# Kernel tuning notes

Hardware: AMD Instinct MI355X
Metric: run time of the kernel (lower is better)

The kernel has to match this reference:

```python
import jax, jax.numpy as jnp
import numpy as np

N = 131072      # nodes decoded per call
LAT, REP, H = 64, 128, 256
FEAT, CEMB, NMAP, CNUM = 512, 128, 101, 27
TEMP = 0.5


def setup_inputs() -> dict:
    key = jax.random.key(0)
    ks = iter(jax.random.split(key, 40))
    w = lambda shape: jax.random.normal(next(ks), shape, jnp.float32) * 0.02
    inp = {
        "z": jax.random.normal(next(ks), (N, LAT), jnp.float32),
        "cluster_ind": jax.random.randint(next(ks), (N,), 0, CNUM),
        "Emb": w((CNUM, CEMB)),
        "Wld": w((LAT, REP)), "bld": w((REP,)),
        "Wrd": w((REP, 3 * H)), "brd": w((3 * H,)),
        "Wfd": w((H, FEAT)), "bfd": w((FEAT,)),
        "Wc1": w((H, H)), "bc1": w((H,)),
        "Wc2": w((H, H)), "bc2": w((H,)),
        "Wc3": w((H, H)), "bc3": w((H,)),
        "Wcd": w((H, CNUM)), "bcd": w((CNUM,)),
        "Wcn": w((CEMB, H)), "bcn": w((H,)),
        "Wnd": w((H, 2 * H)), "bnd": w((2 * H,)),
        "Wn1": w((2 * H, 2 * H)), "bn1": w((2 * H,)),
        "Wn2": w((2 * H, 2 * H)), "bn2": w((2 * H,)),
        "Wa0": w((2 * H, 4 * H)), "ba0": w((4 * H,)),
        "Wa1": w((4 * H, 2 * H)), "ba1": w((2 * H,)),
        "Wn3": w((2 * H, NMAP)), "bn3": w((NMAP,)),
    }
    return inp


def reference(z, cluster_ind, Emb, Wld, bld, Wrd, brd, Wfd, bfd,
              Wc1, bc1, Wc2, bc2, Wc3, bc3, Wcd, bcd, Wcn, bcn,
              Wnd, bnd, Wn1, bn1, Wn2, bn2, Wa0, ba0, Wa1, ba1, Wn3, bn3):
    relu = jax.nn.relu
    # latent -> reparam -> hidden*3, chunked into (feat, neighbor, cluster)
    z1 = relu(z @ Wld + bld)
    z2 = relu(z1 @ Wrd + brd)
    feat_h, nb_h, cl_h = jnp.split(z2, 3, axis=-1)  # each [N, H]
    # feature head
    feat = jax.nn.sigmoid(feat_h @ Wfd + bfd)
    # cluster head
    c = relu(cl_h @ Wc1 + bc1)
    c = relu(c @ Wc2 + bc2)
    c = relu(c @ Wc3 + bc3)
    cluster = jax.nn.sigmoid((c @ Wcd + bcd) / TEMP)
    # neighbor head, conditioned on cluster embedding (training branch)
    emb = Emb[cluster_ind]                      # [N, CEMB]
    ctn = relu(emb @ Wcn + bcn)                 # [N, H]
    nf = relu((nb_h + ctn) @ Wnd + bnd)
    nf = relu(nf @ Wn1 + bn1)
    nf = relu(nf @ Wn2 + bn2)
    nf = relu(nf @ Wa0 + ba0)
    nf = relu(nf @ Wa1 + ba1)
    neighbor_map = jax.nn.sigmoid((nf @ Wn3 + bn3) / TEMP)
    return (feat, neighbor_map, cluster)
```

## Files before the change

### kernel.cpp

```cpp
#include <hip/hip_runtime.h>
#include <hip/hip_bf16.h>

typedef short bf16x8 __attribute__((ext_vector_type(8)));
typedef float f32x4 __attribute__((ext_vector_type(4)));

#define NN 131072
#define BM 128
#define WRS 512
#define SRS 128

#define OFF_LD 0
#define OFF_RD 8192
#define OFF_FD 106496
#define OFF_C1 237568
#define OFF_C2 303104
#define OFF_C3 368640
#define OFF_CD 434176
#define OFF_CN 442368
#define OFF_ND 475136
#define OFF_N1 606208
#define OFF_N2 868352
#define OFF_A0 1130496
#define OFF_A1 1654784
#define OFF_N3 2179072
#define WT_TOTAL 2236416

__device__ __forceinline__ unsigned short f2b(float f) {
  __hip_bfloat16 h = __float2bfloat16(f);
  return __builtin_bit_cast(unsigned short, h);
}
__device__ __forceinline__ float b2f(unsigned short u) {
  return __bfloat162float(__builtin_bit_cast(__hip_bfloat16, u));
}

template<int Kd, int Md>
__device__ __forceinline__ unsigned short convF(int local, const float* __restrict__ W) {
  int block = local >> 9;
  int within = local & 511;
  int lane = within >> 3, j = within & 7;
  constexpr int NK = Kd / 32;
  int ctile = block / NK;
  int kch = block - ctile * NK;
  int col = ctile * 16 + (lane & 15);
  int k = kch * 32 + (lane >> 4) * 8 + j;
  return (col < Md) ? f2b(W[(size_t)k * Md + col]) : (unsigned short)0;
}

__global__ void prep_weights(const float* __restrict__ Wld, const float* __restrict__ Wrd,
                             const float* __restrict__ Wfd, const float* __restrict__ Wc1,
                             const float* __restrict__ Wc2, const float* __restrict__ Wc3,
                             const float* __restrict__ Wcd, const float* __restrict__ Wcn,
                             const float* __restrict__ Wnd, const float* __restrict__ Wn1,
                             const float* __restrict__ Wn2, const float* __restrict__ Wa0,
                             const float* __restrict__ Wa1, const float* __restrict__ Wn3,
                             unsigned short* __restrict__ WT) {
  int e = blockIdx.x * 256 + threadIdx.x;
  unsigned short r;
  if      (e < OFF_RD) r = convF<64, 128>(e - OFF_LD, Wld);
  else if (e < OFF_FD) r = convF<128, 768>(e - OFF_RD, Wrd);
  else if (e < OFF_C1) r = convF<256, 512>(e - OFF_FD, Wfd);
  else if (e < OFF_C2) r = convF<256, 256>(e - OFF_C1, Wc1);
  else if (e < OFF_C3) r = convF<256, 256>(e - OFF_C2, Wc2);
  else if (e < OFF_CD) r = convF<256, 256>(e - OFF_C3, Wc3);
  else if (e < OFF_CN) r = convF<256, 27>(e - OFF_CD, Wcd);
  else if (e < OFF_ND) r = convF<128, 256>(e - OFF_CN, Wcn);
  else if (e < OFF_N1) r = convF<256, 512>(e - OFF_ND, Wnd);
  else if (e < OFF_N2) r = convF<512, 512>(e - OFF_N1, Wn1);
  else if (e < OFF_A0) r = convF<512, 512>(e - OFF_N2, Wn2);
  else if (e < OFF_A1) r = convF<512, 1024>(e - OFF_A0, Wa0);
  else if (e < OFF_N3) r = convF<1024, 512>(e - OFF_A1, Wa1);
  else                 r = convF<512, 101>(e - OFF_N3, Wn3);
  WT[e] = r;
}

template<int K, int NOUT, int GSIZE, int ACT, bool TO_GLOBAL, bool ADD>
__device__ __forceinline__ void layer(
    const unsigned short* __restrict__ Ain, int ars,
    const unsigned short* __restrict__ Bw,
    const float* __restrict__ bias,
    unsigned short* __restrict__ Lout, int ors,
    float* __restrict__ Gout, int gld,
    const unsigned short* __restrict__ Aadd, int rsa,
    int lane, int wid) {
  constexpr int NS = K / 32;
  constexpr int NT = (NOUT + 15) >> 4;
  constexpr int NG = (NT + GSIZE - 1) / GSIZE;
  const int cg = wid >> 1;
  const int rbase = (wid & 1) * 64;
  const int l15 = lane & 15;
  const int quad = lane >> 4;
  const int kh = quad << 3;
  const int sw = (l15 & 7) << 3;
  const unsigned short* ab = Ain + (rbase + l15) * ars;
  #pragma unroll 1
  for (int g = cg; g < NG; g += 4) {
    f32x4 acc[4][GSIZE] = {};
    const unsigned short* bp[GSIZE];
    #pragma unroll
    for (int t = 0; t < GSIZE; ++t) {
      int ti = g * GSIZE + t;
      int tc = ti < NT ? ti : NT - 1;
      bp[t] = Bw + (size_t)tc * (NS * 512) + lane * 8;
    }
    __builtin_amdgcn_s_setprio(1);
    #pragma unroll 2
    for (int s = 0; s < NS; ++s) {
      bf16x8 bb[GSIZE];
      #pragma unroll
      for (int t = 0; t < GSIZE; ++t) bb[t] = *(const bf16x8*)(bp[t] + s * 512);
      int kx = (kh + s * 32) ^ sw;
      #pragma unroll
      for (int m = 0; m < 4; ++m) {
        bf16x8 a = *(const bf16x8*)(ab + m * 16 * ars + kx);
        #pragma unroll
        for (int t = 0; t < GSIZE; ++t)
          acc[m][t] = __builtin_amdgcn_mfma_f32_16x16x32_bf16(a, bb[t], acc[m][t], 0, 0, 0);
      }
    }
    __builtin_amdgcn_s_setprio(0);
    #pragma unroll
    for (int t = 0; t < GSIZE; ++t) {
      int col = (g * GSIZE + t) * 16 + l15;
      int cc = col < NOUT ? col : NOUT - 1;
      float bb2 = bias[cc];
      #pragma unroll
      for (int m = 0; m < 4; ++m) {
        #pragma unroll
        for (int j = 0; j < 4; ++j) {
          int row = rbase + m * 16 + quad * 4 + j;
          int rsw = (row & 7) << 3;
          float v = acc[m][t][j] + bb2;
          if constexpr (ACT == 0) v = fmaxf(v, 0.f);
          else if constexpr (ACT == 1) v = 1.f / (1.f + __expf(-v));
          else if constexpr (ACT == 2) v = 1.f / (1.f + __expf(-2.f * v));
          if constexpr (ADD) v += b2f(Aadd[row * rsa + (col ^ rsw)]);
          if constexpr (TO_GLOBAL) {
            if (col < NOUT) Gout[(size_t)row * gld + col] = v;
          } else {
            Lout[row * ors + (col ^ rsw)] = f2b(v);
          }
        }
      }
    }
  }
}

template<int K>
__device__ __forceinline__ void layer512_ip(
    unsigned short* __restrict__ Wb,
    const unsigned short* __restrict__ Bw, const float* __restrict__ bias,
    int lane, int wid) {
  constexpr int NS = K / 32;
  const int cg = wid >> 1;
  const int rbase = (wid & 1) * 64;
  const int l15 = lane & 15;
  const int quad = lane >> 4;
  const int kh = quad << 3;
  const int sw = (l15 & 7) << 3;
  f32x4 acc[4][8] = {};
  const unsigned short* bp = Bw + (size_t)(cg * 8) * (NS * 512) + lane * 8;
  const unsigned short* ab = Wb + (rbase + l15) * WRS;
  __builtin_amdgcn_s_setprio(1);
  #pragma unroll 2
  for (int s = 0; s < NS; ++s) {
    bf16x8 bb[8];
    #pragma unroll
    for (int t = 0; t < 8; ++t) bb[t] = *(const bf16x8*)(bp + (size_t)t * (NS * 512) + s * 512);
    int kx = (kh + s * 32) ^ sw;
    #pragma unroll
    for (int m = 0; m < 4; ++m) {
      bf16x8 a = *(const bf16x8*)(ab + m * 16 * WRS + kx);
      #pragma unroll
      for (int t = 0; t < 8; ++t)
        acc[m][t] = __builtin_amdgcn_mfma_f32_16x16x32_bf16(a, bb[t], acc[m][t], 0, 0, 0);
    }
  }
  __builtin_amdgcn_s_setprio(0);
  __syncthreads();
  #pragma unroll
  for (int t = 0; t < 8; ++t) {
    int col = cg * 128 + t * 16 + l15;
    float bb2 = bias[col];
    #pragma unroll
    for (int m = 0; m < 4; ++m) {
      #pragma unroll
      for (int j = 0; j < 4; ++j) {
        int row = rbase + m * 16 + quad * 4 + j;
        Wb[row * WRS + (col ^ ((row & 7) << 3))] = f2b(fmaxf(acc[m][t][j] + bb2, 0.f));
      }
    }
  }
  __syncthreads();
}

__global__ __launch_bounds__(512, 2)
void fused_vae(const float* __restrict__ z, const int* __restrict__ cind,
               const float* __restrict__ Emb,
               const float* __restrict__ bld, const float* __restrict__ brd,
               const float* __restrict__ bfd, const float* __restrict__ bc1,
               const float* __restrict__ bc2, const float* __restrict__ bc3,
               const float* __restrict__ bcd, const float* __restrict__ bcn,
               const float* __restrict__ bnd, const float* __restrict__ bn1,
               const float* __restrict__ bn2, const float* __restrict__ ba0,
               const float* __restrict__ ba1, const float* __restrict__ bn3,
               const unsigned short* __restrict__ WT, float* __restrict__ out) {
  __shared__ unsigned short lds[BM * (WRS + SRS)];
  unsigned short* Wb = lds;
  unsigned short* Sb = lds + BM * WRS;
  const int tid = threadIdx.x;
  const int lane = tid & 63;
  const int wid = tid >> 6;
  const size_t row0 = (size_t)blockIdx.x * BM;

  for (int e = tid * 4; e < BM * 64; e += 512 * 4) {
    int r = e >> 6, c = e & 63;
    float4 v = *(const float4*)(z + (row0 + r) * 64 + c);
    ushort4 u; u.x = f2b(v.x); u.y = f2b(v.y); u.z = f2b(v.z); u.w = f2b(v.w);
    *(ushort4*)(&Wb[r * WRS + (c ^ ((r & 7) << 3))]) = u;
  }
  __syncthreads();
  layer<64, 128, 2, 0, false, false>(Wb, WRS, WT + OFF_LD, bld, Sb, SRS, nullptr, 0, nullptr, 0, lane, wid);
  __syncthreads();
  layer<128, 256, 4, 0, false, false>(Sb, SRS, WT + OFF_RD + (size_t)32 * 4 * 512, brd + 512, Wb, WRS, nullptr, 0, nullptr, 0, lane, wid);
  __syncthreads();
  layer<256, 256, 4, 0, false, false>(Wb, WRS, WT + OFF_C1, bc1, Wb + 256, WRS, nullptr, 0, nullptr, 0, lane, wid);
  __syncthreads();
  layer<256, 256, 4, 0, false, false>(Wb + 256, WRS, WT + OFF_C2, bc2, Wb, WRS, nullptr, 0, nullptr, 0, lane, wid);
  __syncthreads();
  layer<256, 256, 4, 0, false, false>(Wb, WRS, WT + OFF_C3, bc3, Wb + 256, WRS, nullptr, 0, nullptr, 0, lane, wid);
  __syncthreads();
  layer<256, 27, 1, 2, true, false>(Wb + 256, WRS, WT + OFF_CD, bcd, nullptr, 0,
                                    out + (size_t)NN * 613 + row0 * 27, 27, nullptr, 0, lane, wid);
  layer<128, 256, 4, 0, false, false>(Sb, SRS, WT + OFF_RD, brd, Wb, WRS, nullptr, 0, nullptr, 0, lane, wid);
  __syncthreads();
  layer<256, 512, 4, 1, true, false>(Wb, WRS, WT + OFF_FD, bfd, nullptr, 0,
                                     out + row0 * 512, 512, nullptr, 0, lane, wid);
  layer<128, 256, 4, 0, false, false>(Sb, SRS, WT + OFF_RD + (size_t)16 * 4 * 512, brd + 256, Wb + 256, WRS, nullptr, 0, nullptr, 0, lane, wid);
  __syncthreads();
  for (int e = tid * 4; e < BM * 128; e += 512 * 4) {
    int r = e >> 7, c = e & 127;
    int ci = cind[row0 + r];
    float4 v = *(const float4*)(Emb + (size_t)ci * 128 + c);
    ushort4 u; u.x = f2b(v.x); u.y = f2b(v.y); u.z = f2b(v.z); u.w = f2b(v.w);
    *(ushort4*)(&Sb[r * SRS + (c ^ ((r & 7) << 3))]) = u;
  }
  __syncthreads();
  layer<128, 256, 4, 0, false, true>(Sb, SRS, WT + OFF_CN, bcn, Wb, WRS, nullptr, 0, Wb + 256, WRS, lane, wid);
  __syncthreads();
  layer512_ip<256>(Wb, WT + OFF_ND, bnd, lane, wid);
  layer512_ip<512>(Wb, WT + OFF_N1, bn1, lane, wid);
  layer512_ip<512>(Wb, WT + OFF_N2, bn2, lane, wid);
  {
    const int l15 = lane & 15;
    const int quad = lane >> 4;
    const int kh = quad << 3;
    const int sw = (l15 & 7) << 3;
    #pragma unroll 1
    for (int rh = 0; rh < 2; ++rh) {
      f32x4 acc1[4][4] = {};
      const unsigned short* awb = Wb + (rh * 64 + l15) * WRS;
      const unsigned short* asb = Sb + l15 * 256;
      #pragma unroll 1
      for (int e = 0; e < 4; ++e) {
        f32x4 acc0[4][2] = {};
        const unsigned short* bp0 = WT + OFF_A0 + (size_t)(e * 16 + wid * 2) * (16 * 512) + lane * 8;
        __builtin_amdgcn_s_setprio(1);
        #pragma unroll 2
        for (int s = 0; s < 16; ++s) {
          bf16x8 b0 = *(const bf16x8*)(bp0 + s * 512);
          bf16x8 b1 = *(const bf16x8*)(bp0 + 16 * 512 + s * 512);
          int kx = (kh + s * 32) ^ sw;
          #pragma unroll
          for (int m = 0; m < 4; ++m) {
            bf16x8 a = *(const bf16x8*)(awb + m * 16 * WRS + kx);
            acc0[m][0] = __builtin_amdgcn_mfma_f32_16x16x32_bf16(a, b0, acc0[m][0], 0, 0, 0);
            acc0[m][1] = __builtin_amdgcn_mfma_f32_16x16x32_bf16(a, b1, acc0[m][1], 0, 0, 0);
          }
        }
        __builtin_amdgcn_s_setprio(0);
        __syncthreads();
        #pragma unroll
        for (int t = 0; t < 2; ++t) {
          int lc = wid * 32 + t * 16 + l15;
          float bb2 = ba0[e * 256 + lc];
          #pragma unroll
          for (int m = 0; m < 4; ++m) {
            #pragma unroll
            for (int j = 0; j < 4; ++j) {
              int row = m * 16 + quad * 4 + j;
              Sb[row * 256 + (lc ^ ((row & 7) << 3))] = f2b(fmaxf(acc0[m][t][j] + bb2, 0.f));
            }
          }
        }
        __syncthreads();
        const unsigned short* bp1 = WT + OFF_A1 + (size_t)(wid * 4) * (32 * 512) + (size_t)(e * 8) * 512 + lane * 8;
        __builtin_amdgcn_s_setprio(1);
        #pragma unroll 2
        for (int s = 0; s < 8; ++s) {
          bf16x8 b[4];
          #pragma unroll
          for (int t = 0; t < 4; ++t) b[t] = *(const bf16x8*)(bp1 + (size_t)t * (32 * 512) + s * 512);
          int kx = (kh + s * 32) ^ sw;
          #pragma unroll
          for (int m = 0; m < 4; ++m) {
            bf16x8 a = *(const bf16x8*)(asb + m * 16 * 256 + kx);
            #pragma unroll
            for (int t = 0; t < 4; ++t)
              acc1[m][t] = __builtin_amdgcn_mfma_f32_16x16x32_bf16(a, b[t], acc1[m][t], 0, 0, 0);
          }
        }
        __builtin_amdgcn_s_setprio(0);
      }
      #pragma unroll
      for (int t = 0; t < 4; ++t) {
        int col = wid * 64 + t * 16 + l15;
        float bb2 = ba1[col];
        #pragma unroll
        for (int m = 0; m < 4; ++m) {
          #pragma unroll
          for (int j = 0; j < 4; ++j) {
            int row = rh * 64 + m * 16 + quad * 4 + j;
            Wb[row * WRS + (col ^ ((row & 7) << 3))] = f2b(fmaxf(acc1[m][t][j] + bb2, 0.f));
          }
        }
      }
    }
  }
  __syncthreads();
  layer<512, 101, 2, 2, true, false>(Wb, WRS, WT + OFF_N3, bn3, nullptr, 0,
                                     out + (size_t)NN * 512 + row0 * 101, 101, nullptr, 0, lane, wid);
}

extern "C" void kernel_launch(void* const* d_in, const int* in_sizes, int n_in,
                              void* d_out, int out_size, void* d_ws, size_t ws_size,
                              hipStream_t stream) {
  const float* z   = (const float*)d_in[0];
  const int*   cind= (const int*)d_in[1];
  const float* Emb = (const float*)d_in[2];
  const float* Wld = (const float*)d_in[3];  const float* bld = (const float*)d_in[4];
  const float* Wrd = (const float*)d_in[5];  const float* brd = (const float*)d_in[6];
  const float* Wfd = (const float*)d_in[7];  const float* bfd = (const float*)d_in[8];
  const float* Wc1 = (const float*)d_in[9];  const float* bc1 = (const float*)d_in[10];
  const float* Wc2 = (const float*)d_in[11]; const float* bc2 = (const float*)d_in[12];
  const float* Wc3 = (const float*)d_in[13]; const float* bc3 = (const float*)d_in[14];
  const float* Wcd = (const float*)d_in[15]; const float* bcd = (const float*)d_in[16];
  const float* Wcn = (const float*)d_in[17]; const float* bcn = (const float*)d_in[18];
  const float* Wnd = (const float*)d_in[19]; const float* bnd = (const float*)d_in[20];
  const float* Wn1 = (const float*)d_in[21]; const float* bn1 = (const float*)d_in[22];
  const float* Wn2 = (const float*)d_in[23]; const float* bn2 = (const float*)d_in[24];
  const float* Wa0 = (const float*)d_in[25]; const float* ba0 = (const float*)d_in[26];
  const float* Wa1 = (const float*)d_in[27]; const float* ba1 = (const float*)d_in[28];
  const float* Wn3 = (const float*)d_in[29]; const float* bn3 = (const float*)d_in[30];
  unsigned short* WT = (unsigned short*)d_ws;
  float* out = (float*)d_out;

  prep_weights<<<WT_TOTAL / 256, 256, 0, stream>>>(Wld, Wrd, Wfd, Wc1, Wc2, Wc3, Wcd,
                                                   Wcn, Wnd, Wn1, Wn2, Wa0, Wa1, Wn3, WT);
  fused_vae<<<NN / BM, 512, 0, stream>>>(z, cind, Emb, bld, brd, bfd, bc1, bc2, bc3,
                                         bcd, bcn, bnd, bn1, bn2, ba0, ba1, bn3, WT, out);
}
```

Baseline: 660.9 us.

## Switch wide neighbor-head layers to 32x32x16 MFMA tiles with repacked weights

```diff
diff --git a/kernel.cpp b/kernel.cpp
--- a/kernel.cpp
+++ b/kernel.cpp
@@ -3,6 +3,7 @@
 
 typedef short bf16x8 __attribute__((ext_vector_type(8)));
 typedef float f32x4 __attribute__((ext_vector_type(4)));
+typedef float f32x16 __attribute__((ext_vector_type(16)));
 
 #define NN 131072
 #define BM 128
@@ -44,6 +45,19 @@
   int col = ctile * 16 + (lane & 15);
   int k = kch * 32 + (lane >> 4) * 8 + j;
   return (col < Md) ? f2b(W[(size_t)k * Md + col]) : (unsigned short)0;
+}
+
+template<int Kd, int Md>
+__device__ __forceinline__ unsigned short convF32(int local, const float* __restrict__ W) {
+  int block = local >> 9;
+  int within = local & 511;
+  int lane = within >> 3, j = within & 7;
+  constexpr int NK = Kd / 16;
+  int ctile = block / NK;
+  int kch = block - ctile * NK;
+  int col = ctile * 32 + (lane & 31);
+  int k = kch * 16 + (lane >> 5) * 8 + j;
+  return f2b(W[(size_t)k * Md + col]);
 }
 
 __global__ void prep_weights(const float* __restrict__ Wld, const float* __restrict__ Wrd,
@@ -64,11 +78,11 @@
   else if (e < OFF_CD) r = convF<256, 256>(e - OFF_C3, Wc3);
   else if (e < OFF_CN) r = convF<256, 27>(e - OFF_CD, Wcd);
   else if (e < OFF_ND) r = convF<128, 256>(e - OFF_CN, Wcn);
-  else if (e < OFF_N1) r = convF<256, 512>(e - OFF_ND, Wnd);
-  else if (e < OFF_N2) r = convF<512, 512>(e - OFF_N1, Wn1);
-  else if (e < OFF_A0) r = convF<512, 512>(e - OFF_N2, Wn2);
-  else if (e < OFF_A1) r = convF<512, 1024>(e - OFF_A0, Wa0);
-  else if (e < OFF_N3) r = convF<1024, 512>(e - OFF_A1, Wa1);
+  else if (e < OFF_N1) r = convF32<256, 512>(e - OFF_ND, Wnd);
+  else if (e < OFF_N2) r = convF32<512, 512>(e - OFF_N1, Wn1);
+  else if (e < OFF_A0) r = convF32<512, 512>(e - OFF_N2, Wn2);
+  else if (e < OFF_A1) r = convF32<512, 1024>(e - OFF_A0, Wa0);
+  else if (e < OFF_N3) r = convF32<1024, 512>(e - OFF_A1, Wa1);
   else                 r = convF<512, 101>(e - OFF_N3, Wn3);
   WT[e] = r;
 }
@@ -150,43 +164,42 @@
     unsigned short* __restrict__ Wb,
     const unsigned short* __restrict__ Bw, const float* __restrict__ bias,
     int lane, int wid) {
-  constexpr int NS = K / 32;
+  constexpr int NS = K / 16;
   const int cg = wid >> 1;
   const int rbase = (wid & 1) * 64;
-  const int l15 = lane & 15;
-  const int quad = lane >> 4;
-  const int kh = quad << 3;
-  const int sw = (l15 & 7) << 3;
-  f32x4 acc[4][8] = {};
-  const unsigned short* bp = Bw + (size_t)(cg * 8) * (NS * 512) + lane * 8;
-  const unsigned short* ab = Wb + (rbase + l15) * WRS;
+  const int l31 = lane & 31;
+  const int kh32 = (lane >> 5) << 3;
+  const int sw32 = (lane & 7) << 3;
+  f32x16 acc[2][4] = {};
+  const unsigned short* bp = Bw + (size_t)(cg * 4) * (NS * 512) + lane * 8;
+  const unsigned short* ab = Wb + (rbase + l31) * WRS;
   __builtin_amdgcn_s_setprio(1);
   #pragma unroll 2
   for (int s = 0; s < NS; ++s) {
-    bf16x8 bb[8];
-    #pragma unroll
-    for (int t = 0; t < 8; ++t) bb[t] = *(const bf16x8*)(bp + (size_t)t * (NS * 512) + s * 512);
-    int kx = (kh + s * 32) ^ sw;
-    #pragma unroll
-    for (int m = 0; m < 4; ++m) {
-      bf16x8 a = *(const bf16x8*)(ab + m * 16 * WRS + kx);
-      #pragma unroll
-      for (int t = 0; t < 8; ++t)
-        acc[m][t] = __builtin_amdgcn_mfma_f32_16x16x32_bf16(a, bb[t], acc[m][t], 0, 0, 0);
+    bf16x8 bb[4];
+    #pragma unroll
+    for (int t = 0; t < 4; ++t) bb[t] = *(const bf16x8*)(bp + (size_t)t * (NS * 512) + s * 512);
+    int kx = (kh32 + s * 16) ^ sw32;
+    #pragma unroll
+    for (int rt = 0; rt < 2; ++rt) {
+      bf16x8 a = *(const bf16x8*)(ab + rt * 32 * WRS + kx);
+      #pragma unroll
+      for (int t = 0; t < 4; ++t)
+        acc[rt][t] = __builtin_amdgcn_mfma_f32_32x32x16_bf16(a, bb[t], acc[rt][t], 0, 0, 0);
     }
   }
   __builtin_amdgcn_s_setprio(0);
   __syncthreads();
   #pragma unroll
-  for (int t = 0; t < 8; ++t) {
-    int col = cg * 128 + t * 16 + l15;
+  for (int t = 0; t < 4; ++t) {
+    int col = cg * 128 + t * 32 + l31;
     float bb2 = bias[col];
     #pragma unroll
-    for (int m = 0; m < 4; ++m) {
-      #pragma unroll
-      for (int j = 0; j < 4; ++j) {
-        int row = rbase + m * 16 + quad * 4 + j;
-        Wb[row * WRS + (col ^ ((row & 7) << 3))] = f2b(fmaxf(acc[m][t][j] + bb2, 0.f));
+    for (int rt = 0; rt < 2; ++rt) {
+      #pragma unroll
+      for (int r = 0; r < 16; ++r) {
+        int row = rbase + rt * 32 + (r & 3) + 8 * (r >> 2) + 4 * (lane >> 5);
+        Wb[row * WRS + (col ^ ((row & 7) << 3))] = f2b(fmaxf(acc[rt][t][r] + bb2, 0.f));
       }
     }
   }
@@ -251,76 +264,69 @@
   layer512_ip<512>(Wb, WT + OFF_N1, bn1, lane, wid);
   layer512_ip<512>(Wb, WT + OFF_N2, bn2, lane, wid);
   {
-    const int l15 = lane & 15;
-    const int quad = lane >> 4;
-    const int kh = quad << 3;
-    const int sw = (l15 & 7) << 3;
+    const int l31 = lane & 31;
+    const int kh32 = (lane >> 5) << 3;
+    const int sw32 = (lane & 7) << 3;
+    const int irh = wid & 1;
+    const int cga = wid >> 1;
     #pragma unroll 1
     for (int rh = 0; rh < 2; ++rh) {
-      f32x4 acc1[4][4] = {};
-      const unsigned short* awb = Wb + (rh * 64 + l15) * WRS;
-      const unsigned short* asb = Sb + l15 * 256;
+      f32x16 acc1[2][2] = {};
+      const unsigned short* awb0 = Wb + (rh * 64 + irh * 32 + l31) * WRS;
+      const unsigned short* asb = Sb + l31 * 256;
       #pragma unroll 1
       for (int e = 0; e < 4; ++e) {
-        f32x4 acc0[4][2] = {};
-        const unsigned short* bp0 = WT + OFF_A0 + (size_t)(e * 16 + wid * 2) * (16 * 512) + lane * 8;
+        f32x16 acc0[2] = {};
+        const unsigned short* bp0 = WT + OFF_A0 + (size_t)(e * 8 + cga * 2) * (32 * 512) + lane * 8;
+        __builtin_amdgcn_s_setprio(1);
+        #pragma unroll 2
+        for (int s = 0; s < 32; ++s) {
+          bf16x8 b0 = *(const bf16x8*)(bp0 + s * 512);
+          bf16x8 b1 = *(const bf16x8*)(bp0 + 32 * 512 + s * 512);
+          int kx = (kh32 + s * 16) ^ sw32;
+          bf16x8 a = *(const bf16x8*)(awb0 + kx);
+          acc0[0] = __builtin_amdgcn_mfma_f32_32x32x16_bf16(a, b0, acc0[0], 0, 0, 0);
+          acc0[1] = __builtin_amdgcn_mfma_f32_32x32x16_bf16(a, b1, acc0[1], 0, 0, 0);
+        }
+        __builtin_amdgcn_s_setprio(0);
+        __syncthreads();
+        #pragma unroll
+        for (int ct = 0; ct < 2; ++ct) {
+          int lc = cga * 64 + ct * 32 + l31;
+          float bb2 = ba0[e * 256 + lc];
+          #pragma unroll
+          for (int r = 0; r < 16; ++r) {
+            int row = irh * 32 + (r & 3) + 8 * (r >> 2) + 4 * (lane >> 5);
+            Sb[row * 256 + (lc ^ ((row & 7) << 3))] = f2b(fmaxf(acc0[ct][r] + bb2, 0.f));
+          }
+        }
+        __syncthreads();
+        const unsigned short* bp1 = WT + OFF_A1 + (size_t)(wid * 2) * (64 * 512) + (size_t)(e * 16) * 512 + lane * 8;
         __builtin_amdgcn_s_setprio(1);
         #pragma unroll 2
         for (int s = 0; s < 16; ++s) {
-          bf16x8 b0 = *(const bf16x8*)(bp0 + s * 512);
-          bf16x8 b1 = *(const bf16x8*)(bp0 + 16 * 512 + s * 512);
-          int kx = (kh + s * 32) ^ sw;
+          bf16x8 b0 = *(const bf16x8*)(bp1 + s * 512);
+          bf16x8 b1 = *(const bf16x8*)(bp1 + 64 * 512 + s * 512);
+          int kx = (kh32 + s * 16) ^ sw32;
           #pragma unroll
-          for (int m = 0; m < 4; ++m) {
-            bf16x8 a = *(const bf16x8*)(awb + m * 16 * WRS + kx);
-            acc0[m][0] = __builtin_amdgcn_mfma_f32_16x16x32_bf16(a, b0, acc0[m][0], 0, 0, 0);
-            acc0[m][1] = __builtin_amdgcn_mfma_f32_16x16x32_bf16(a, b1, acc0[m][1], 0, 0, 0);
+          for (int rt = 0; rt < 2; ++rt) {
+            bf16x8 a = *(const bf16x8*)(asb + rt * 32 * 256 + kx);
+            acc1[rt][0] = __builtin_amdgcn_mfma_f32_32x32x16_bf16(a, b0, acc1[rt][0], 0, 0, 0);
+            acc1[rt][1] = __builtin_amdgcn_mfma_f32_32x32x16_bf16(a, b1, acc1[rt][1], 0, 0, 0);
           }
         }
         __builtin_amdgcn_s_setprio(0);
-        __syncthreads();
+      }
+      #pragma unroll
+      for (int rt = 0; rt < 2; ++rt) {
         #pragma unroll
-        for (int t = 0; t < 2; ++t) {
-          int lc = wid * 32 + t * 16 + l15;
-          float bb2 = ba0[e * 256 + lc];
+        for (int ct = 0; ct < 2; ++ct) {
+          int col = wid * 64 + ct * 32 + l31;
+          float bb2 = ba1[col];
           #pragma unroll
-          for (int m = 0; m < 4; ++m) {
-            #pragma unroll
-            for (int j = 0; j < 4; ++j) {
-              int row = m * 16 + quad * 4 + j;
-              Sb[row * 256 + (lc ^ ((row & 7) << 3))] = f2b(fmaxf(acc0[m][t][j] + bb2, 0.f));
-            }
-          }
-        }
-        __syncthreads();
-        const unsigned short* bp1 = WT + OFF_A1 + (size_t)(wid * 4) * (32 * 512) + (size_t)(e * 8) * 512 + lane * 8;
-        __builtin_amdgcn_s_setprio(1);
-        #pragma unroll 2
-        for (int s = 0; s < 8; ++s) {
-          bf16x8 b[4];
-          #pragma unroll
-          for (int t = 0; t < 4; ++t) b[t] = *(const bf16x8*)(bp1 + (size_t)t * (32 * 512) + s * 512);
-          int kx = (kh + s * 32) ^ sw;
-          #pragma unroll
-          for (int m = 0; m < 4; ++m) {
-            bf16x8 a = *(const bf16x8*)(asb + m * 16 * 256 + kx);
-            #pragma unroll
-            for (int t = 0; t < 4; ++t)
-              acc1[m][t] = __builtin_amdgcn_mfma_f32_16x16x32_bf16(a, b[t], acc1[m][t], 0, 0, 0);
-          }
-        }
-        __builtin_amdgcn_s_setprio(0);
-      }
-      #pragma unroll
-      for (int t = 0; t < 4; ++t) {
-        int col = wid * 64 + t * 16 + l15;
-        float bb2 = ba1[col];
-        #pragma unroll
-        for (int m = 0; m < 4; ++m) {
-          #pragma unroll
-          for (int j = 0; j < 4; ++j) {
-            int row = rh * 64 + m * 16 + quad * 4 + j;
-            Wb[row * WRS + (col ^ ((row & 7) << 3))] = f2b(fmaxf(acc1[m][t][j] + bb2, 0.f));
+          for (int r = 0; r < 16; ++r) {
+            int row = rh * 64 + rt * 32 + (r & 3) + 8 * (r >> 2) + 4 * (lane >> 5);
+            Wb[row * WRS + (col ^ ((row & 7) << 3))] = f2b(fmaxf(acc1[rt][ct][r] + bb2, 0.f));
           }
         }
       }
```

Measured after the change: 790.1 us. 1.2x slower.
